# Optimization experiments

Hardware: AMD Instinct MI355X
Metric: run time of the kernel (lower is better)

## Reference

```python
import jax, jax.numpy as jnp
import numpy as np

K = 161  # frequency bins
T = 2000  # time frames
M_INIT = 5.0  # initial triangular window width (args.m)


def setup_inputs() -> dict:
    key = jax.random.key(0)
    k1, k2 = jax.random.split(key)
    # learned window-width parameter, initialized near args.m with small jitter
    m = M_INIT + 0.5 * jax.random.normal(k1, (K, T, 1), dtype=jnp.float32)
    # spectrogram input, indexed as input[0, 0, :, :] in the original
    x = jax.random.normal(k2, (1, 1, K, T), dtype=jnp.float32)
    input_length = T
    return {"m": m, "x": x, "input_length": input_length}


def reference(m, x, input_length):
    # m: (K, T, 1) learned param; x: (1, 1, K, T) spectrogram.
    k = m.shape[0]
    am = jnp.abs(m)[:, :, 0]                      # (K, T)  == abs_m broadcast
    idx = jnp.arange(k, dtype=jnp.float32)
    # |range1 - range2|[i, t, j] = |j - i|, independent of t -> (K, K)
    d = jnp.abs(idx[None, :] - idx[:, None])      # d[i, j] = |j - i|
    wide = am > 1.0                               # (K, T) window-vs-delta mask
    # triangular window: relu(|m| - |j-i|) / m^2 (safe denom where branch unused)
    am2 = jnp.where(wide, am * am, 1.0)
    tri = jax.nn.relu(am[:, :, None] - d[:, None, :]) / am2[:, :, None]  # (K,T,K)
    delta = jnp.eye(k, dtype=jnp.float32)[:, None, :]                    # (i==j)
    blar = jnp.where(wide[:, :, None], tri, delta)                       # (K,T,K)
    blar = blar / jnp.sum(blar, axis=2, keepdims=True)                   # normalize over j
    # out[j, t] = sum_i blar[i, t, j] * x[i, t]
    xs = x[0, 0]                                  # (K, T)
    smoothed = jnp.einsum('itj,it->jt', blar, xs)  # (K, T)
    return smoothed.reshape(1, 1, k, xs.shape[1])
```

## Files before the change

kernel.cpp:

```cpp
#include <hip/hip_runtime.h>

#define KBINS 161
#define TFRAMES 2000
#define TILE_T 4

__global__ __launch_bounds__(256) void m_noise_smooth_kernel(
    const float* __restrict__ m,
    const float* __restrict__ x,
    float* __restrict__ out) {
  const int t0 = blockIdx.x * TILE_T;
  const int tid = threadIdx.x;

  __shared__ float s_am[KBINS * TILE_T];
  __shared__ float s_scale[KBINS * TILE_T];
  __shared__ float s_x[KBINS * TILE_T];
  __shared__ float s_wmax[4];

  float thread_max = 0.0f;

  if (tid < KBINS) {
    const int i = tid;
    const float4 vx = *(const float4*)(x + i * TFRAMES + t0);
    *(float4*)(s_x + i * TILE_T) = vx;

    const float4 vm = *(const float4*)(m + i * TFRAMES + t0);
    const float vv[4] = {vm.x, vm.y, vm.z, vm.w};
#pragma unroll
    for (int e = 0; e < 4; ++e) {
      const float am = fabsf(vv[e]);
      thread_max = fmaxf(thread_max, am);
      float S = am;
      int dmax = (int)am;
      if (dmax > KBINS - 1) dmax = KBINS - 1;
      for (int d = 1; d <= dmax; ++d) {
        const int cnt = (i - d >= 0) + (i + d < KBINS);
        S += (am - (float)d) * (float)cnt;
      }
      s_am[i * TILE_T + e] = am;
      s_scale[i * TILE_T + e] = (am > 1.0f) ? (1.0f / S) : 0.0f;
    }
  }

#pragma unroll
  for (int off = 32; off > 0; off >>= 1)
    thread_max = fmaxf(thread_max, __shfl_xor(thread_max, off, 64));
  if ((tid & 63) == 0) s_wmax[tid >> 6] = thread_max;
  __syncthreads();
  const float maxam =
      fmaxf(fmaxf(s_wmax[0], s_wmax[1]), fmaxf(s_wmax[2], s_wmax[3]));
  int R = (int)ceilf(maxam);
  if (R > KBINS - 1) R = KBINS - 1;

  const int t_ = tid & 3;
  for (int j = (tid >> 2); j < KBINS; j += 64) {
    const int lo = (j - R > 0) ? (j - R) : 0;
    const int hi = (j + R < KBINS - 1) ? (j + R) : (KBINS - 1);
    const float sc_j = s_scale[j * TILE_T + t_];
    float acc = (sc_j == 0.0f) ? s_x[j * TILE_T + t_] : 0.0f;
    for (int i = lo; i <= hi; ++i) {
      const float w =
          fmaxf(s_am[i * TILE_T + t_] - fabsf((float)(j - i)), 0.0f) *
          s_scale[i * TILE_T + t_];
      acc = fmaf(w, s_x[i * TILE_T + t_], acc);
    }
    out[j * TFRAMES + t0 + t_] = acc;
  }
}

extern "C" void kernel_launch(void* const* d_in, const int* in_sizes, int n_in,
                              void* d_out, int out_size, void* d_ws, size_t ws_size,
                              hipStream_t stream) {
  const float* m = (const float*)d_in[0];
  const float* x = (const float*)d_in[1];
  float* out = (float*)d_out;

  m_noise_smooth_kernel<<<TFRAMES / TILE_T, 256, 0, stream>>>(m, x, out);
}
```

Before: 66.33 us.

## Split into prep and gather kernels with closed-form window normalization

Replaces the per-element serial loop that sums the triangular window with a closed-form arithmetic-series expression. A prep kernel writes (|m|, x/S) pairs to workspace along with per-tile maxima of |m|. A gather kernel then computes each output from coalesced global loads over a band of radius R, using a finer block granularity across j and t. This removes the O(|m|) loop and the poorly coalesced 4-frame tiles, at the cost of an extra launch and a workspace round trip. The delta branch is folded in as A=1, G=x.

New measurement: 65.34 us. Within noise of the previous version (-1.5%).

```diff
diff --git a/kernel.cpp b/kernel.cpp
--- a/kernel.cpp
+++ b/kernel.cpp
@@ -2,77 +2,101 @@
 
 #define KBINS 161
 #define TFRAMES 2000
-#define TILE_T 4
+#define KT_PAD 322048
+#define NTBLK 8
+#define JT 4
+#define TT 64
 
-__global__ __launch_bounds__(256) void m_noise_smooth_kernel(
+__global__ __launch_bounds__(256) void m_noise_prep_kernel(
     const float* __restrict__ m,
     const float* __restrict__ x,
-    float* __restrict__ out) {
-  const int t0 = blockIdx.x * TILE_T;
-  const int tid = threadIdx.x;
+    float2* __restrict__ AG,
+    float* __restrict__ M1) {
+  const int i = blockIdx.x;
+  const int tblk = blockIdx.y;
+  const int t = tblk * 256 + threadIdx.x;
+  const bool valid = (t < TFRAMES);
 
-  __shared__ float s_am[KBINS * TILE_T];
-  __shared__ float s_scale[KBINS * TILE_T];
-  __shared__ float s_x[KBINS * TILE_T];
-  __shared__ float s_wmax[4];
+  float Av = 0.0f;
+  if (valid) {
+    const float mv = m[i * TFRAMES + t];
+    const float xv = x[i * TFRAMES + t];
+    const float am = fabsf(mv);
+    const bool wide = am > 1.0f;
 
-  float thread_max = 0.0f;
+    const float fD = floorf(fminf(am, (float)KBINS));
+    const float fa = fminf((float)i, fD);
+    const float fb = fminf((float)(KBINS - 1 - i), fD);
+    const float DD = fD * (fD + 1.0f);
+    const float F0 = fD * am - 0.5f * DD;
+    const float Fa = (fD - fa) * am - 0.5f * (DD - fa * (fa + 1.0f));
+    const float Fb = (fD - fb) * am - 0.5f * (DD - fb * (fb + 1.0f));
+    const float S = am + 2.0f * F0 - Fa - Fb;
 
-  if (tid < KBINS) {
-    const int i = tid;
-    const float4 vx = *(const float4*)(x + i * TFRAMES + t0);
-    *(float4*)(s_x + i * TILE_T) = vx;
-
-    const float4 vm = *(const float4*)(m + i * TFRAMES + t0);
-    const float vv[4] = {vm.x, vm.y, vm.z, vm.w};
-#pragma unroll
-    for (int e = 0; e < 4; ++e) {
-      const float am = fabsf(vv[e]);
-      thread_max = fmaxf(thread_max, am);
-      float S = am;
-      int dmax = (int)am;
-      if (dmax > KBINS - 1) dmax = KBINS - 1;
-      for (int d = 1; d <= dmax; ++d) {
-        const int cnt = (i - d >= 0) + (i + d < KBINS);
-        S += (am - (float)d) * (float)cnt;
-      }
-      s_am[i * TILE_T + e] = am;
-      s_scale[i * TILE_T + e] = (am > 1.0f) ? (1.0f / S) : 0.0f;
-    }
+    Av = wide ? am : 1.0f;
+    const float Gv = wide ? xv / S : xv;
+    AG[i * TFRAMES + t] = make_float2(Av, Gv);
   }
 
+  float rm = Av;
 #pragma unroll
-  for (int off = 32; off > 0; off >>= 1)
-    thread_max = fmaxf(thread_max, __shfl_xor(thread_max, off, 64));
-  if ((tid & 63) == 0) s_wmax[tid >> 6] = thread_max;
+  for (int off = 32; off; off >>= 1) rm = fmaxf(rm, __shfl_xor(rm, off, 64));
+  __shared__ float s_red[4];
+  if ((threadIdx.x & 63) == 0) s_red[threadIdx.x >> 6] = rm;
   __syncthreads();
-  const float maxam =
-      fmaxf(fmaxf(s_wmax[0], s_wmax[1]), fmaxf(s_wmax[2], s_wmax[3]));
-  int R = (int)ceilf(maxam);
+  if (threadIdx.x == 0)
+    M1[tblk * KBINS + i] =
+        fmaxf(fmaxf(s_red[0], s_red[1]), fmaxf(s_red[2], s_red[3]));
+}
+
+__global__ __launch_bounds__(256) void m_noise_gather_kernel(
+    const float2* __restrict__ AG, const float* __restrict__ M1,
+    float* __restrict__ out) {
+  const int tid = threadIdx.x;
+  const int j = blockIdx.x * JT + (tid >> 6);
+  const int t = blockIdx.y * TT + (tid & 63);
+  const int tblk = blockIdx.y >> 2;
+
+  float mv = (tid < KBINS) ? M1[tblk * KBINS + tid] : 0.0f;
+#pragma unroll
+  for (int off = 32; off; off >>= 1) mv = fmaxf(mv, __shfl_xor(mv, off, 64));
+  __shared__ float s_red[4];
+  if ((tid & 63) == 0) s_red[tid >> 6] = mv;
+  __syncthreads();
+  const float maxA =
+      fmaxf(fmaxf(s_red[0], s_red[1]), fmaxf(s_red[2], s_red[3]));
+  int R = (int)ceilf(maxA);
+  if (R < 1) R = 1;
   if (R > KBINS - 1) R = KBINS - 1;
 
-  const int t_ = tid & 3;
-  for (int j = (tid >> 2); j < KBINS; j += 64) {
+  if (j < KBINS) {
     const int lo = (j - R > 0) ? (j - R) : 0;
     const int hi = (j + R < KBINS - 1) ? (j + R) : (KBINS - 1);
-    const float sc_j = s_scale[j * TILE_T + t_];
-    float acc = (sc_j == 0.0f) ? s_x[j * TILE_T + t_] : 0.0f;
+    const float2* p = AG + (size_t)lo * TFRAMES + t;
+    float fd = (float)(j - lo);
+    float acc = 0.0f;
+#pragma unroll 4
     for (int i = lo; i <= hi; ++i) {
-      const float w =
-          fmaxf(s_am[i * TILE_T + t_] - fabsf((float)(j - i)), 0.0f) *
-          s_scale[i * TILE_T + t_];
-      acc = fmaf(w, s_x[i * TILE_T + t_], acc);
+      const float2 ag = *p;
+      acc = fmaf(fmaxf(ag.x - fabsf(fd), 0.0f), ag.y, acc);
+      fd -= 1.0f;
+      p += TFRAMES;
     }
-    out[j * TFRAMES + t0 + t_] = acc;
+    if (t < TFRAMES) out[j * TFRAMES + t] = acc;
   }
 }
 
 extern "C" void kernel_launch(void* const* d_in, const int* in_sizes, int n_in,
-                              void* d_out, int out_size, void* d_ws, size_t ws_size,
-                              hipStream_t stream) {
+                              void* d_out, int out_size, void* d_ws,
+                              size_t ws_size, hipStream_t stream) {
   const float* m = (const float*)d_in[0];
   const float* x = (const float*)d_in[1];
   float* out = (float*)d_out;
 
-  m_noise_smooth_kernel<<<TFRAMES / TILE_T, 256, 0, stream>>>(m, x, out);
+  float2* AG = (float2*)d_ws;
+  float* M1 = (float*)d_ws + 2 * (size_t)KT_PAD;
+
+  m_noise_prep_kernel<<<dim3(KBINS, NTBLK), 256, 0, stream>>>(m, x, AG, M1);
+  m_noise_gather_kernel<<<dim3((KBINS + JT - 1) / JT, (TFRAMES + TT - 1) / TT),
+                          256, 0, stream>>>(AG, M1, out);
 }
```
